# Kernel optimization log

Measured on AMD Instinct MI355X. Metric: run time of the kernel, lower is better.

The kernel has to match this reference:

```python
import jax, jax.numpy as jnp
import numpy as np

TOKENS = 16384
HIDDEN = 2048
GROUP_SIZE = 128
EPS = 1e-05
FP8_MAX = 448.0  # float8_e4m3fn max


def rmsnorm(x, w, eps=EPS):
    # vLLM RMSNorm: x * rsqrt(mean(x^2)) * weight
    var = jnp.mean(x * x, axis=-1, keepdims=True)
    return x * jax.lax.rsqrt(var + eps) * w


def fused_add_rmsnorm(x, residual, w, eps=EPS):
    # vLLM RMSNorm(x, residual): residual += x; out = rmsnorm(residual)
    resid = x + residual
    return rmsnorm(resid, w, eps), resid


def per_token_group_quant_fp8_ue8m0(y, group_size=GROUP_SIZE):
    # QuantFP8(static=False, group_shape=(1,128), use_ue8m0=True)
    t, h = y.shape
    g = y.reshape(t, h // group_size, group_size)
    amax = jnp.max(jnp.abs(g), axis=-1)                      # [T, H/G]
    scale = jnp.maximum(amax, 1e-10) / FP8_MAX
    scale = jnp.exp2(jnp.ceil(jnp.log2(scale)))              # ue8m0: round scale up to power of 2
    q = jnp.clip(g / scale[..., None], -FP8_MAX, FP8_MAX)
    q = q.astype(jnp.float8_e4m3fn)                          # fp8 rounding
    return q.reshape(t, h), scale


def setup_inputs() -> dict:
    key = jax.random.key(0)
    kx, kw = jax.random.split(key)
    x = jax.random.normal(kx, (TOKENS, HIDDEN), dtype=jnp.float32)
    norm_w = jnp.ones((4, HIDDEN), dtype=jnp.float32)
    w = jax.random.uniform(kw, (3, HIDDEN, HIDDEN), dtype=jnp.float32)
    return {"x": x, "norm_w": norm_w, "w": w}


def reference(x, norm_w, w):
    # tensor_model_parallel_all_reduce == identity at world_size 1
    z = jax.nn.relu(x)
    xr = z
    resid = z
    y = rmsnorm(xr, norm_w[0])
    x2 = y @ w[0]
    y2, resid = fused_add_rmsnorm(x2, resid, norm_w[1])
    y2_q, y2_s = per_token_group_quant_fp8_ue8m0(y2)
    x3 = y2_q.astype(x.dtype) @ w[1]
    y3, resid = fused_add_rmsnorm(x3, resid, norm_w[2])
    y3_q, y3_s = per_token_group_quant_fp8_ue8m0(y3)
    x4 = y3_q.astype(x.dtype) @ w[2]
    y4, resid = fused_add_rmsnorm(x4, resid, norm_w[3])
    return (y4, y2_s, y3_s)
```

## Files before the change

kernel.cpp:

```cpp
#include <hip/hip_runtime.h>
#include <stdint.h>
#include <math.h>

#define NTOK 16384
#define HID  2048
#define NGRP 16
#define EPSF 1e-5f

typedef __bf16 bf16;
typedef __bf16 bf16x8 __attribute__((ext_vector_type(8)));
typedef float  f32x4  __attribute__((ext_vector_type(4)));


__device__ __forceinline__ void async_load16(const void* g, void* l) {
  __builtin_amdgcn_global_load_lds((const __attribute__((address_space(1))) void*)g,
                                   (__attribute__((address_space(3))) void*)l, 16, 0, 0);
}

__device__ __forceinline__ float fp8_e4m3_rne(float v) {
  float a = fabsf(v);
  float s = (v < 0.f) ? -1.f : 1.f;
  if (a < 0.015625f) {
    float r = rintf(a * 512.0f);
    return s * r * 0.001953125f;
  }
  uint32_t u = __float_as_uint(a);
  u = (u + 0x7FFFFu + ((u >> 20) & 1u)) & 0xFFF00000u;
  return s * __uint_as_float(u);
}

__device__ __forceinline__ float block_sum256(float v) {
  __shared__ float sh[4];
  #pragma unroll
  for (int o = 32; o > 0; o >>= 1) v += __shfl_xor(v, o, 64);
  if ((threadIdx.x & 63) == 0) sh[threadIdx.x >> 6] = v;
  __syncthreads();
  return sh[0] + sh[1] + sh[2] + sh[3];
}

__device__ __forceinline__ float ue8m0_scale(float amax) {
  float v = fmaxf(amax, 1e-10f) / 448.0f;
  float l = (float)log2((double)v);
  return exp2f(ceilf(l));
}


__global__ __launch_bounds__(256) void k_transpose_cast(const float* __restrict__ W,
                                                        bf16* __restrict__ Wt) {
  __shared__ float tile[64][65];
  const size_t mat = (size_t)HID * HID;
  const float* Wz = W + mat * blockIdx.z;
  bf16* Wtz = Wt + mat * blockIdx.z;
  int bn = blockIdx.x * 64;
  int bk = blockIdx.y * 64;
  int t = threadIdx.x;
  {
    int r = t >> 4, c = (t & 15) * 4;
    #pragma unroll
    for (int i = 0; i < 4; i++) {
      float4 v = *(const float4*)(Wz + (size_t)(bk + r + 16 * i) * HID + bn + c);
      tile[r + 16 * i][c] = v.x; tile[r + 16 * i][c + 1] = v.y;
      tile[r + 16 * i][c + 2] = v.z; tile[r + 16 * i][c + 3] = v.w;
    }
  }
  __syncthreads();
  {
    int n = t >> 2, kc = (t & 3) * 16;
    bf16x8 o0, o1;
    #pragma unroll
    for (int j = 0; j < 8; j++) o0[j] = (bf16)tile[kc + j][n];
    #pragma unroll
    for (int j = 0; j < 8; j++) o1[j] = (bf16)tile[kc + 8 + j][n];
    bf16* dst = Wtz + (size_t)(bn + n) * HID + bk + kc;
    *(bf16x8*)dst = o0;
    *(bf16x8*)(dst + 8) = o1;
  }
}

__global__ __launch_bounds__(256) void k_pre(const float* __restrict__ x,
                                             const float* __restrict__ nw,
                                             bf16* __restrict__ Y,
                                             bf16* __restrict__ R) {
  size_t base = (size_t)blockIdx.x * HID + threadIdx.x * 8;
  float4 v0 = *(const float4*)(x + base);
  float4 v1 = *(const float4*)(x + base + 4);
  float z[8] = {v0.x, v0.y, v0.z, v0.w, v1.x, v1.y, v1.z, v1.w};
  float ss = 0.f;
  #pragma unroll
  for (int i = 0; i < 8; i++) { z[i] = fmaxf(z[i], 0.f); ss += z[i] * z[i]; }
  float tot = block_sum256(ss);
  float s = rsqrtf(tot * (1.0f / HID) + EPSF);
  bf16x8 rr;
  #pragma unroll
  for (int i = 0; i < 8; i++) rr[i] = (bf16)z[i];
  *(bf16x8*)(R + base) = rr;
  int j0 = threadIdx.x * 8;
  float4 w0 = *(const float4*)(nw + j0);
  float4 w1 = *(const float4*)(nw + j0 + 4);
  float wv[8] = {w0.x, w0.y, w0.z, w0.w, w1.x, w1.y, w1.z, w1.w};
  bf16x8 o;
  #pragma unroll
  for (int i = 0; i < 8; i++) o[i] = (bf16)(z[i] * s * wv[i]);
  *(bf16x8*)(Y + base) = o;
}

__global__ __launch_bounds__(256) void k_fuse_quant(const bf16* __restrict__ residIn,
                                                    const bf16* __restrict__ Cin,
                                                    const float* __restrict__ nw,
                                                    bf16* __restrict__ residOut,
                                                    bf16* __restrict__ Aout,
                                                    float* __restrict__ scaleOut) {
  int row = blockIdx.x;
  int j0 = threadIdx.x * 8;
  size_t base = (size_t)row * HID + j0;
  bf16x8 c  = *(const bf16x8*)(Cin + base);
  bf16x8 rv = *(const bf16x8*)(residIn + base);
  float r[8]; float ss = 0.f;
  #pragma unroll
  for (int i = 0; i < 8; i++) { r[i] = (float)rv[i] + (float)c[i]; ss += r[i] * r[i]; }
  float tot = block_sum256(ss);
  float s = rsqrtf(tot * (1.0f / HID) + EPSF);

  bf16x8 ro;
  #pragma unroll
  for (int i = 0; i < 8; i++) ro[i] = (bf16)r[i];
  *(bf16x8*)(residOut + base) = ro;

  float4 w0 = *(const float4*)(nw + j0);
  float4 w1 = *(const float4*)(nw + j0 + 4);
  float wv[8] = {w0.x, w0.y, w0.z, w0.w, w1.x, w1.y, w1.z, w1.w};
  float y[8], amax = 0.f;
  #pragma unroll
  for (int i = 0; i < 8; i++) { y[i] = r[i] * s * wv[i]; amax = fmaxf(amax, fabsf(y[i])); }
  amax = fmaxf(amax, __shfl_xor(amax, 1, 64));
  amax = fmaxf(amax, __shfl_xor(amax, 2, 64));
  amax = fmaxf(amax, __shfl_xor(amax, 4, 64));
  amax = fmaxf(amax, __shfl_xor(amax, 8, 64));
  float scale = ue8m0_scale(amax);
  float inv = 1.0f / scale;
  bf16x8 q;
  #pragma unroll
  for (int i = 0; i < 8; i++) {
    float t = fminf(fmaxf(y[i] * inv, -448.f), 448.f);
    q[i] = (bf16)fp8_e4m3_rne(t);
  }
  *(bf16x8*)(Aout + base) = q;
  if ((threadIdx.x & 15) == 0) scaleOut[(size_t)row * NGRP + (j0 >> 7)] = scale;
}

__global__ __launch_bounds__(256) void k_final(const bf16* __restrict__ residIn,
                                               const bf16* __restrict__ Cin,
                                               const float* __restrict__ nw,
                                               float* __restrict__ out) {
  size_t base = (size_t)blockIdx.x * HID + threadIdx.x * 8;
  bf16x8 c  = *(const bf16x8*)(Cin + base);
  bf16x8 rv = *(const bf16x8*)(residIn + base);
  float r[8]; float ss = 0.f;
  #pragma unroll
  for (int i = 0; i < 8; i++) { r[i] = (float)rv[i] + (float)c[i]; ss += r[i] * r[i]; }
  float tot = block_sum256(ss);
  float s = rsqrtf(tot * (1.0f / HID) + EPSF);
  int j0 = threadIdx.x * 8;
  float4 w0 = *(const float4*)(nw + j0);
  float4 w1 = *(const float4*)(nw + j0 + 4);
  float wv[8] = {w0.x, w0.y, w0.z, w0.w, w1.x, w1.y, w1.z, w1.w};
  float4 o0, o1;
  o0.x = r[0]*s*wv[0]; o0.y = r[1]*s*wv[1]; o0.z = r[2]*s*wv[2]; o0.w = r[3]*s*wv[3];
  o1.x = r[4]*s*wv[4]; o1.y = r[5]*s*wv[5]; o1.z = r[6]*s*wv[6]; o1.w = r[7]*s*wv[7];
  *(float4*)(out + base) = o0;
  *(float4*)(out + base + 4) = o1;
}

__global__ __launch_bounds__(256) void k_gemm(const bf16* __restrict__ A,
                                              const bf16* __restrict__ B,
                                              bf16* __restrict__ C,
                                              int M, int N, int K) {
  __shared__ __align__(16) bf16 As[128 * 64];
  __shared__ __align__(16) bf16 Bs[128 * 64];
  int b = blockIdx.x;
  int xcd = b & 7, j = b >> 3;
  int bn = xcd * 2 + (j & 1);
  int bm = j >> 1;
  int tid = threadIdx.x;
  int wave = tid >> 6, lane = tid & 63;
  int q = lane >> 4, rr = lane & 15;

  const bf16* Aq[4]; const bf16* Bq[4];
  #pragma unroll
  for (int i = 0; i < 4; i++) {
    int s  = wave * 256 + i * 64 + lane;
    int r  = s >> 3, c = s & 7;
    int gc = c ^ ((r >> 1) & 7);
    Aq[i] = A + (size_t)(bm * 128 + r) * K + gc * 8;
    Bq[i] = B + (size_t)(bn * 128 + r) * K + gc * 8;
  }
  char* AsB = (char*)As;
  char* BsB = (char*)Bs;

  f32x4 acc[4][4];
  #pragma unroll
  for (int mi = 0; mi < 4; mi++)
    #pragma unroll
    for (int ni = 0; ni < 4; ni++)
      #pragma unroll
      for (int e = 0; e < 4; e++) acc[mi][ni][e] = 0.f;

  int m_off = (wave >> 1) * 64;
  int n_off = (wave & 1) * 64;
  int swz = (rr >> 1) & 7;

  int arow[4], brow[4];
  #pragma unroll
  for (int i = 0; i < 4; i++) {
    arow[i] = (m_off + i * 16 + rr) * 64;
    brow[i] = (n_off + i * 16 + rr) * 64;
  }

  for (int k0 = 0; k0 < K; k0 += 64) {
    __syncthreads();
    #pragma unroll
    for (int i = 0; i < 4; i++)
      async_load16(Aq[i] + k0, AsB + wave * 4096 + i * 1024);
    #pragma unroll
    for (int i = 0; i < 4; i++)
      async_load16(Bq[i] + k0, BsB + wave * 4096 + i * 1024);
    __syncthreads();

    #pragma unroll
    for (int ms = 0; ms < 2; ms++) {
      int p = ((ms * 4 + q) ^ swz) * 8;
      bf16x8 af[4], bfr[4];
      #pragma unroll
      for (int mi = 0; mi < 4; mi++)
        af[mi] = *(const bf16x8*)(As + arow[mi] + p);
      #pragma unroll
      for (int ni = 0; ni < 4; ni++)
        bfr[ni] = *(const bf16x8*)(Bs + brow[ni] + p);
      #pragma unroll
      for (int mi = 0; mi < 4; mi++)
        #pragma unroll
        for (int ni = 0; ni < 4; ni++)
          acc[mi][ni] = __builtin_amdgcn_mfma_f32_16x16x32_bf16(af[mi], bfr[ni], acc[mi][ni], 0, 0, 0);
    }
  }

  #pragma unroll
  for (int mi = 0; mi < 4; mi++)
    #pragma unroll
    for (int ni = 0; ni < 4; ni++)
      #pragma unroll
      for (int t = 0; t < 4; t++) {
        int rowi = bm * 128 + m_off + mi * 16 + q * 4 + t;
        int coli = bn * 128 + n_off + ni * 16 + rr;
        C[(size_t)rowi * N + coli] = (bf16)acc[mi][ni][t];
      }
}


extern "C" void kernel_launch(void* const* d_in, const int* in_sizes, int n_in,
                              void* d_out, int out_size, void* d_ws, size_t ws_size,
                              hipStream_t stream) {
  const float* x      = (const float*)d_in[0];
  const float* norm_w = (const float*)d_in[1];
  const float* w      = (const float*)d_in[2];

  float* out   = (float*)d_out;
  float* y4o   = out;
  float* s2o   = out + (size_t)NTOK * HID;
  float* s3o   = s2o + (size_t)NTOK * NGRP;

  char* ws = (char*)d_ws;
  const size_t WT_B = (size_t)3 * HID * HID * 2;
  const size_t AB_B = (size_t)NTOK * HID * 2;
  bf16* Wt   = (bf16*)ws;
  bf16* Abuf = (bf16*)(ws + WT_B);
  bf16* Cbuf = (bf16*)(ws + WT_B + AB_B);
  bf16* Rbuf = (bf16*)(ws + WT_B + 2 * AB_B);
  const size_t MATE = (size_t)HID * HID;

  dim3 gT(HID / 64, HID / 64, 3);
  int  gG = (HID / 128) * (NTOK / 128);

  k_transpose_cast<<<gT, 256, 0, stream>>>(w, Wt);
  k_pre<<<NTOK, 256, 0, stream>>>(x, norm_w, Abuf, Rbuf);
  k_gemm<<<gG, 256, 0, stream>>>(Abuf, Wt, Cbuf, NTOK, HID, HID);
  k_fuse_quant<<<NTOK, 256, 0, stream>>>(Rbuf, Cbuf, norm_w + HID, Rbuf, Abuf, s2o);
  k_gemm<<<gG, 256, 0, stream>>>(Abuf, Wt + MATE, Cbuf, NTOK, HID, HID);
  k_fuse_quant<<<NTOK, 256, 0, stream>>>(Rbuf, Cbuf, norm_w + 2 * HID, Rbuf, Abuf, s3o);
  k_gemm<<<gG, 256, 0, stream>>>(Abuf, Wt + 2 * MATE, Cbuf, NTOK, HID, HID);
  k_final<<<NTOK, 256, 0, stream>>>(Rbuf, Cbuf, norm_w + 3 * HID, y4o);
}
```

Baseline: 795.6 us.

## Rewrite GEMM as 256x256 tile with 4-stage async LDS pipeline

Replaces the 128x128, 256-thread GEMM with a 256x256 tile computed by 512 threads (8 waves, 128x64 per wave). Operands stream through a 4-deep ring of LDS buffers via async global-to-LDS loads with explicit vmcnt waits, so loads overlap with MFMA work. It also splits each K-step into two half-phases with raised scheduling priority around the MFMAs. Larger tiles cut global traffic per flop. The costs are heavy register pressure (128 accumulator floats per thread), 128 KB of LDS, and fewer blocks (512) to cover the CUs.

```diff
diff --git a/kernel.cpp b/kernel.cpp
--- a/kernel.cpp
+++ b/kernel.cpp
@@ -15,6 +15,12 @@
 __device__ __forceinline__ void async_load16(const void* g, void* l) {
   __builtin_amdgcn_global_load_lds((const __attribute__((address_space(1))) void*)g,
                                    (__attribute__((address_space(3))) void*)l, 16, 0, 0);
+}
+
+__device__ __forceinline__ void bar() {
+  asm volatile("" ::: "memory");
+  __builtin_amdgcn_s_barrier();
+  asm volatile("" ::: "memory");
 }
 
 __device__ __forceinline__ float fp8_e4m3_rne(float v) {
@@ -171,88 +177,107 @@
   *(float4*)(out + base + 4) = o1;
 }
 
-__global__ __launch_bounds__(256) void k_gemm(const bf16* __restrict__ A,
-                                              const bf16* __restrict__ B,
-                                              bf16* __restrict__ C,
-                                              int M, int N, int K) {
-  __shared__ __align__(16) bf16 As[128 * 64];
-  __shared__ __align__(16) bf16 Bs[128 * 64];
+__global__ __launch_bounds__(512, 2) void k_gemm(const bf16* __restrict__ A,
+                                                 const bf16* __restrict__ B,
+                                                 bf16* __restrict__ C,
+                                                 int M, int N, int K) {
+  __shared__ __align__(16) char lds[4 * 32768];
   int b = blockIdx.x;
-  int xcd = b & 7, j = b >> 3;
-  int bn = xcd * 2 + (j & 1);
-  int bm = j >> 1;
+  int bn = b & 7;
+  int bm = b >> 3;
   int tid = threadIdx.x;
   int wave = tid >> 6, lane = tid & 63;
   int q = lane >> 4, rr = lane & 15;
-
-  const bf16* Aq[4]; const bf16* Bq[4];
-  #pragma unroll
-  for (int i = 0; i < 4; i++) {
-    int s  = wave * 256 + i * 64 + lane;
-    int r  = s >> 3, c = s & 7;
-    int gc = c ^ ((r >> 1) & 7);
-    Aq[i] = A + (size_t)(bm * 128 + r) * K + gc * 8;
-    Bq[i] = B + (size_t)(bn * 128 + r) * K + gc * 8;
-  }
-  char* AsB = (char*)As;
-  char* BsB = (char*)Bs;
-
-  f32x4 acc[4][4];
-  #pragma unroll
-  for (int mi = 0; mi < 4; mi++)
-    #pragma unroll
-    for (int ni = 0; ni < 4; ni++)
+  int wm = wave >> 2, wn = wave & 3;
+
+  const bf16* aSrc[2]; const bf16* bSrc[2];
+  #pragma unroll
+  for (int i = 0; i < 2; i++) {
+    int m = i * 512 + tid;
+    int r = m >> 2;
+    int c = (m & 3) ^ ((r >> 1) & 3);
+    aSrc[i] = A + (size_t)(bm * 256 + r) * K + c * 8;
+    bSrc[i] = B + (size_t)(bn * 256 + r) * K + c * 8;
+  }
+
+  const int swz = (rr >> 1) & 3;
+  const int ldoff = rr * 64 + ((q ^ swz) << 4);
+
+  f32x4 acc[8][4];
+  #pragma unroll
+  for (int mf = 0; mf < 8; mf++)
+    #pragma unroll
+    for (int nf = 0; nf < 4; nf++)
       #pragma unroll
-      for (int e = 0; e < 4; e++) acc[mi][ni][e] = 0.f;
-
-  int m_off = (wave >> 1) * 64;
-  int n_off = (wave & 1) * 64;
-  int swz = (rr >> 1) & 7;
-
-  int arow[4], brow[4];
-  #pragma unroll
-  for (int i = 0; i < 4; i++) {
-    arow[i] = (m_off + i * 16 + rr) * 64;
-    brow[i] = (n_off + i * 16 + rr) * 64;
-  }
-
-  for (int k0 = 0; k0 < K; k0 += 64) {
-    __syncthreads();
-    #pragma unroll
-    for (int i = 0; i < 4; i++)
-      async_load16(Aq[i] + k0, AsB + wave * 4096 + i * 1024);
-    #pragma unroll
-    for (int i = 0; i < 4; i++)
-      async_load16(Bq[i] + k0, BsB + wave * 4096 + i * 1024);
-    __syncthreads();
-
-    #pragma unroll
-    for (int ms = 0; ms < 2; ms++) {
-      int p = ((ms * 4 + q) ^ swz) * 8;
-      bf16x8 af[4], bfr[4];
+      for (int e = 0; e < 4; e++) acc[mf][nf][e] = 0.f;
+
+  const int NT = K / 32;
+
+  #pragma unroll
+  for (int t = 0; t < 3; ++t) {
+    char* db = lds + t * 32768 + wave * 1024;
+    async_load16(aSrc[0] + t * 32, db);
+    async_load16(aSrc[1] + t * 32, db + 8192);
+    async_load16(bSrc[0] + t * 32, db + 16384);
+    async_load16(bSrc[1] + t * 32, db + 16384 + 8192);
+  }
+  asm volatile("s_waitcnt vmcnt(8)" ::: "memory");
+  bar();
+
+  for (int t = 0; t < NT; ++t) {
+    const char* sb  = lds + (t & 3) * 32768;
+    const char* rbA = sb + wm * 8192 + ldoff;
+    const char* rbB = sb + 16384 + wn * 4096 + ldoff;
+    const int u  = (t + 3 < NT) ? (t + 3) : (NT - 1);
+    char* ub = lds + ((t + 3) & 3) * 32768 + wave * 1024;
+
+    bf16x8 bfr[4], afr[4];
+    #pragma unroll
+    for (int nf = 0; nf < 4; nf++)
+      bfr[nf] = *(const bf16x8*)(rbB + nf * 1024);
+    #pragma unroll
+    for (int mf = 0; mf < 4; mf++)
+      afr[mf] = *(const bf16x8*)(rbA + mf * 1024);
+    async_load16(aSrc[0] + u * 32, ub);
+    async_load16(aSrc[1] + u * 32, ub + 8192);
+    bar();
+    __builtin_amdgcn_s_setprio(1);
+    #pragma unroll
+    for (int mf = 0; mf < 4; mf++)
       #pragma unroll
-      for (int mi = 0; mi < 4; mi++)
-        af[mi] = *(const bf16x8*)(As + arow[mi] + p);
+      for (int nf = 0; nf < 4; nf++)
+        acc[mf][nf] = __builtin_amdgcn_mfma_f32_16x16x32_bf16(afr[mf], bfr[nf], acc[mf][nf], 0, 0, 0);
+    __builtin_amdgcn_s_setprio(0);
+    bar();
+
+    #pragma unroll
+    for (int mf = 0; mf < 4; mf++)
+      afr[mf] = *(const bf16x8*)(rbA + 4096 + mf * 1024);
+    async_load16(bSrc[0] + u * 32, ub + 16384);
+    async_load16(bSrc[1] + u * 32, ub + 16384 + 8192);
+    bar();
+    __builtin_amdgcn_s_setprio(1);
+    #pragma unroll
+    for (int mf = 0; mf < 4; mf++)
       #pragma unroll
-      for (int ni = 0; ni < 4; ni++)
-        bfr[ni] = *(const bf16x8*)(Bs + brow[ni] + p);
+      for (int nf = 0; nf < 4; nf++)
+        acc[4 + mf][nf] = __builtin_amdgcn_mfma_f32_16x16x32_bf16(afr[mf], bfr[nf], acc[4 + mf][nf], 0, 0, 0);
+    __builtin_amdgcn_s_setprio(0);
+    asm volatile("s_waitcnt vmcnt(8)" ::: "memory");
+    bar();
+  }
+
+  asm volatile("s_waitcnt vmcnt(0)" ::: "memory");
+
+  #pragma unroll
+  for (int mf = 0; mf < 8; mf++)
+    #pragma unroll
+    for (int nf = 0; nf < 4; nf++)
       #pragma unroll
-      for (int mi = 0; mi < 4; mi++)
-        #pragma unroll
-        for (int ni = 0; ni < 4; ni++)
-          acc[mi][ni] = __builtin_amdgcn_mfma_f32_16x16x32_bf16(af[mi], bfr[ni], acc[mi][ni], 0, 0, 0);
-    }
-  }
-
-  #pragma unroll
-  for (int mi = 0; mi < 4; mi++)
-    #pragma unroll
-    for (int ni = 0; ni < 4; ni++)
-      #pragma unroll
-      for (int t = 0; t < 4; t++) {
-        int rowi = bm * 128 + m_off + mi * 16 + q * 4 + t;
-        int coli = bn * 128 + n_off + ni * 16 + rr;
-        C[(size_t)rowi * N + coli] = (bf16)acc[mi][ni][t];
+      for (int tt = 0; tt < 4; tt++) {
+        int rowi = bm * 256 + wm * 128 + mf * 16 + q * 4 + tt;
+        int coli = bn * 256 + wn * 64 + nf * 16 + rr;
+        C[(size_t)rowi * N + coli] = (bf16)acc[mf][nf][tt];
       }
 }
 
@@ -279,14 +304,14 @@
   const size_t MATE = (size_t)HID * HID;
 
   dim3 gT(HID / 64, HID / 64, 3);
-  int  gG = (HID / 128) * (NTOK / 128);
+  int  gG = (NTOK / 256) * (HID / 256);
 
   k_transpose_cast<<<gT, 256, 0, stream>>>(w, Wt);
   k_pre<<<NTOK, 256, 0, stream>>>(x, norm_w, Abuf, Rbuf);
-  k_gemm<<<gG, 256, 0, stream>>>(Abuf, Wt, Cbuf, NTOK, HID, HID);
+  k_gemm<<<gG, 512, 0, stream>>>(Abuf, Wt, Cbuf, NTOK, HID, HID);
   k_fuse_quant<<<NTOK, 256, 0, stream>>>(Rbuf, Cbuf, norm_w + HID, Rbuf, Abuf, s2o);
-  k_gemm<<<gG, 256, 0, stream>>>(Abuf, Wt + MATE, Cbuf, NTOK, HID, HID);
+  k_gemm<<<gG, 512, 0, stream>>>(Abuf, Wt + MATE, Cbuf, NTOK, HID, HID);
   k_fuse_quant<<<NTOK, 256, 0, stream>>>(Rbuf, Cbuf, norm_w + 2 * HID, Rbuf, Abuf, s3o);
-  k_gemm<<<gG, 256, 0, stream>>>(Abuf, Wt + 2 * MATE, Cbuf, NTOK, HID, HID);
+  k_gemm<<<gG, 512, 0, stream>>>(Abuf, Wt + 2 * MATE, Cbuf, NTOK, HID, HID);
   k_final<<<NTOK, 256, 0, stream>>>(Rbuf, Cbuf, norm_w + 3 * HID, y4o);
 }
```

Measured after the change: 788.8 us. Within noise of the previous version (-0.9%).
